# Optimization experiments

Hardware: AMD Instinct MI355X
Metric: run time of the kernel (lower is better)

## Reference

```python
import jax, jax.numpy as jnp
import numpy as np
from jax import lax

# ---- configuration (matches init_kwargs) ----
DH = 4.0        # grid_spacing (m)
DT = 0.0008     # time step (s), satisfies CFL for vmax=2600
PML = 20        # pml_width (cells, all four edges)
VMAX = 2600.0   # max_vel used for PML profile
PAD = 2         # halo for 4th-order (accuracy=4) stencil


def _shift(wp, k, axis, n):
    return lax.slice_in_dim(wp, PAD + k, PAD + k + n, axis=axis)


def _d1(w, axis, dh):
    # 4th-order first derivative: (-f[+2] + 8 f[+1] - 8 f[-1] + f[-2]) / (12 h)
    n = w.shape[axis]
    pad = [(0, 0)] * w.ndim
    pad[axis] = (PAD, PAD)
    wp = jnp.pad(w, pad)
    return ((_shift(wp, -2, axis, n) - _shift(wp, 2, axis, n))
            + 8.0 * (_shift(wp, 1, axis, n) - _shift(wp, -1, axis, n))) / (12.0 * dh)


def _d2(w, axis, dh):
    # 4th-order second derivative: (-f[+-2] + 16 f[+-1] - 30 f[0]) / (12 h^2)
    n = w.shape[axis]
    pad = [(0, 0)] * w.ndim
    pad[axis] = (PAD, PAD)
    wp = jnp.pad(w, pad)
    return (-(_shift(wp, -2, axis, n) + _shift(wp, 2, axis, n))
            + 16.0 * (_shift(wp, 1, axis, n) + _shift(wp, -1, axis, n))
            - 30.0 * w) / (12.0 * dh * dh)


def _pml_profiles(n, pml, dh, dt, vmax):
    # CPML absorption profiles: sigma ~ quadratic ramp into the PML,
    # b = exp(-sigma*dt), a = b - 1 (kappa=1, alpha=0)
    sigma_max = np.float32(3.0 * vmax * np.log(1000.0) / (2.0 * pml * dh))
    x = jnp.arange(n, dtype=jnp.float32)
    d = jnp.maximum(jnp.clip((pml - x) / pml, 0.0, 1.0),
                    jnp.clip((x - (n - 1 - pml)) / pml, 0.0, 1.0))
    sigma = sigma_max * d * d
    b = jnp.exp(-sigma * dt)
    return b - 1.0, b


def setup_inputs() -> dict:
    key = jax.random.key(0)
    k1, k2, k3, k4 = jax.random.split(key, 4)
    ny = nx = 400
    B, n_src, n_rec, nt = 4, 1, 100, 100
    v = 1500.0 + 1000.0 * jax.random.uniform(k1, (ny, nx), dtype=jnp.float32)
    source_amplitudes = jax.random.normal(k2, (B, n_src, nt), dtype=jnp.float32)
    source_locations = jax.random.randint(k3, (B, n_src, 2), 40, 360).astype(jnp.int64)
    receiver_locations = jax.random.randint(k4, (B, n_rec, 2), 40, 360).astype(jnp.int64)
    return {"v": v, "source_amplitudes": source_amplitudes,
            "source_locations": source_locations,
            "receiver_locations": receiver_locations}


def reference(v, source_amplitudes, source_locations, receiver_locations):
    B, n_src, nt = source_amplitudes.shape
    # replicate edge velocities into the PML region (as deepwave does)
    vp = jnp.pad(v, ((PML, PML), (PML, PML)), mode="edge")
    NY, NX = vp.shape
    v2dt2 = (vp * vp) * (DT * DT)          # [NY, NX]
    ay, by = _pml_profiles(NY, PML, DH, DT, VMAX)
    ax, bx = _pml_profiles(NX, PML, DH, DT, VMAX)
    ay, by = ay[None, :, None], by[None, :, None]
    ax, bx = ax[None, None, :], bx[None, None, :]

    sy = source_locations[..., 0] + PML    # [B, n_src]
    sx = source_locations[..., 1] + PML
    ry = receiver_locations[..., 0] + PML  # [B, n_rec]
    rx = receiver_locations[..., 1] + PML
    bidx = jnp.arange(B)[:, None]
    src_scale = v2dt2[sy, sx]              # [B, n_src]

    zero = jnp.zeros((B, NY, NX), v.dtype)
    carry0 = (zero, zero, zero, zero, zero, zero)

    def step(carry, amp_t):
        wfc, wfm, psiy, psix, zetay, zetax = carry
        # PML memory variables for first derivatives
        psiy = by * psiy + ay * _d1(wfc, 1, DH)
        psix = bx * psix + ax * _d1(wfc, 2, DH)
        # PML-corrected second derivatives
        d2y = _d2(wfc, 1, DH) + _d1(psiy, 1, DH)
        d2x = _d2(wfc, 2, DH) + _d1(psix, 2, DH)
        zetay = by * zetay + ay * d2y
        zetax = bx * zetax + ax * d2x
        # explicit leapfrog time step
        wfp = v2dt2[None] * (d2y + zetay + d2x + zetax) + 2.0 * wfc - wfm
        # inject sources scaled by v^2 dt^2 (as deepwave)
        wfp = wfp.at[bidx, sy, sx].add(src_scale * amp_t)
        rec = wfp[bidx, ry, rx]            # [B, n_rec]
        return (wfp, wfc, psiy, psix, zetay, zetax), rec

    amps_t = jnp.moveaxis(source_amplitudes, 2, 0)  # [nt, B, n_src]
    _, recs = lax.scan(step, carry0, amps_t)        # recs: [nt, B, n_rec]
    receiver_amplitudes = jnp.moveaxis(recs, 0, 2)  # [B, n_rec, nt]
    return receiver_amplitudes
```

## Files before the change

kernel.cpp:

```cpp
#include <hip/hip_runtime.h>

#define NVEL  400
#define PMLW  20
#define NSIDE 440
#define BATCH 4
#define NT    100
#define NREC  100

#define TS 55
#define GT 8
#define WP 65
#define PYP 56
#define PXP 60
#define ZP  56

#define C1f (1.0f/48.0f)
#define C2f (1.0f/192.0f)
#define NTH 1024

#define WIDX(y,x) (((y)+4)*WP + ((x)+4))

__global__ __launch_bounds__(NTH, 1) void kWave(
    const float* __restrict__ v, const float* __restrict__ amp,
    const int* __restrict__ sloc, const int* __restrict__ rloc,
    float* __restrict__ out, int* __restrict__ flags, float* __restrict__ strips)
{
    __shared__ float sWF0[63*WP], sWF1[63*WP];
    __shared__ float sPY[59*PYP];
    __shared__ float sPX[TS*PXP];
    __shared__ float sZY[TS*ZP], sZX[TS*ZP], sV2[TS*ZP];
    __shared__ float pa_y[63], pb_y[63], pa_x[63], pb_x[63];
    __shared__ float sAmp[NT];

    const int tid  = threadIdx.x;
    const int lane = tid & 63;
    const int wrow = tid >> 6;
    const int bid = blockIdx.x;
    const int b   = bid >> 6;
    const int tl  = bid & 63;
    const int tyi = tl >> 3, txi = tl & 7;
    const int by0 = tyi*TS, bx0 = txi*TS;
    const int nbN = (tyi > 0)    ? bid - GT : -1;
    const int nbS = (tyi < GT-1) ? bid + GT : -1;
    const int nbW = (txi > 0)    ? bid - 1  : -1;
    const int nbE = (txi < GT-1) ? bid + 1  : -1;

    for (int i = tid; i < 63*WP; i += NTH) { sWF0[i] = 0.f; sWF1[i] = 0.f; }
    for (int i = tid; i < 59*PYP; i += NTH) sPY[i] = 0.f;
    for (int i = tid; i < TS*PXP; i += NTH) sPX[i] = 0.f;
    for (int i = tid; i < TS*ZP; i += NTH) { sZY[i] = 0.f; sZX[i] = 0.f; }
    for (int i = tid; i < TS*TS; i += NTH) {
        int y = i/TS, x = i - y*TS;
        int cy = min(max(by0 + y - PMLW, 0), NVEL-1);
        int cx = min(max(bx0 + x - PMLW, 0), NVEL-1);
        float vv = v[cy*NVEL + cx];
        sV2[y*ZP + x] = vv*vv*(float)(0.0008*0.0008);
    }
    if (tid < 63) {
        const float smax = (float)(3.0*2600.0*6.907755278982137/160.0);
        float gy = (float)(by0 + tid - 4);
        float dy = fmaxf(fminf(fmaxf((20.f-gy)/20.f,0.f),1.f),
                         fminf(fmaxf((gy-419.f)/20.f,0.f),1.f));
        float bby = expf(-smax*dy*dy*0.0008f);
        pb_y[tid] = bby; pa_y[tid] = bby - 1.f;
        float gx = (float)(bx0 + tid - 4);
        float dx = fmaxf(fminf(fmaxf((20.f-gx)/20.f,0.f),1.f),
                         fminf(fmaxf((gx-419.f)/20.f,0.f),1.f));
        float bbx = expf(-smax*dx*dx*0.0008f);
        pb_x[tid] = bbx; pa_x[tid] = bbx - 1.f;
    }
    if (tid < NT) sAmp[tid] = amp[b*NT + tid];

    const int sly = sloc[b*2]   + PMLW - by0;
    const int slx = sloc[b*2+1] + PMLW - bx0;

    int rofs = -1, rIdx = 0;
    if (tid < NREC) {
        int gry = rloc[(b*NREC+tid)*2]   + PMLW;
        int grx = rloc[(b*NREC+tid)*2+1] + PMLW;
        if (gry >= by0 && gry < by0+TS && grx >= bx0 && grx < bx0+TS) {
            rofs = (b*NREC+tid)*NT;
            rIdx = WIDX(gry-by0, grx-bx0);
        }
    }

    int imp_nb = -1, imp_src = 0, imp_dst = 0, exp_src = 0;
    if (tid < 880) {
        int e = tid/220, j = tid - e*220;
        if (e == 0)      { int r=j/55, c=j-55*r; imp_nb=nbN; imp_src=1*220+j; imp_dst=WIDX(r-4,c);   exp_src=WIDX(r,c); }
        else if (e == 1) { int r=j/55, c=j-55*r; imp_nb=nbS; imp_src=0*220+j; imp_dst=WIDX(55+r,c);  exp_src=WIDX(51+r,c); }
        else if (e == 2) { int r=j&3,  c=j>>2;   imp_nb=nbW; imp_src=3*220+j; imp_dst=WIDX(c,r-4);   exp_src=WIDX(c,r); }
        else             { int r=j&3,  c=j>>2;   imp_nb=nbE; imp_src=2*220+j; imp_dst=WIDX(c,55+r);  exp_src=WIDX(c,51+r); }
    }
    __syncthreads();

    float* cur = sWF0;
    float* nxt = sWF1;

    for (int t = 0; t < NT; ++t) {
        if (t > 0 && imp_nb >= 0) {
            int spin = 0;
            while (__hip_atomic_load(&flags[imp_nb], __ATOMIC_RELAXED,
                                     __HIP_MEMORY_SCOPE_AGENT) < t
                   && spin < 2000000) { __builtin_amdgcn_s_sleep(1); ++spin; }
            asm volatile("" ::: "memory");
            cur[imp_dst] = __hip_atomic_load(
                &strips[(size_t)(((t-1)&1)*256 + imp_nb)*880 + imp_src],
                __ATOMIC_RELAXED, __HIP_MEMORY_SCOPE_AGENT);
        }
        __syncthreads();

        #pragma unroll
        for (int k = 0; k < 4; ++k) {
            int ri = wrow + 16*k;
            if (ri < 59 && lane < 55) {
                int r = ri - 2;
                int w = WIDX(r, lane);
                float d1 = (cur[w-2*WP] - cur[w+2*WP]
                            + 8.f*(cur[w+WP] - cur[w-WP])) * C1f;
                int gy = by0 + r;
                int pi = ri*PYP + lane;
                float val = 0.f;
                if (gy >= 0 && gy < NSIDE)
                    val = pb_y[r+4]*sPY[pi] + pa_y[r+4]*d1;
                sPY[pi] = val;
            }
        }
        #pragma unroll
        for (int k = 0; k < 4; ++k) {
            int y = wrow + 16*k;
            if (y < 55 && lane < 59) {
                int c = lane - 2;
                int w = WIDX(y, c);
                float d1 = (cur[w-2] - cur[w+2]
                            + 8.f*(cur[w+1] - cur[w-1])) * C1f;
                int gx = bx0 + c;
                int pi = y*PXP + lane;
                float val = 0.f;
                if (gx >= 0 && gx < NSIDE)
                    val = pb_x[c+4]*sPX[pi] + pa_x[c+4]*d1;
                sPX[pi] = val;
            }
        }
        __syncthreads();

        #pragma unroll
        for (int k = 0; k < 4; ++k) {
            int y = wrow + 16*k;
            if (y < 55 && lane < 55) {
                int x = lane;
                int w = WIDX(y, x);
                float wc = cur[w];
                float d2y = (-(cur[w-2*WP] + cur[w+2*WP])
                             + 16.f*(cur[w-WP] + cur[w+WP]) - 30.f*wc) * C2f
                          + (sPY[y*PYP+x] - sPY[(y+4)*PYP+x]
                             + 8.f*(sPY[(y+3)*PYP+x] - sPY[(y+1)*PYP+x])) * C1f;
                float d2x = (-(cur[w-2] + cur[w+2])
                             + 16.f*(cur[w-1] + cur[w+1]) - 30.f*wc) * C2f
                          + (sPX[y*PXP+x] - sPX[y*PXP+x+4]
                             + 8.f*(sPX[y*PXP+x+3] - sPX[y*PXP+x+1])) * C1f;
                int zi = y*ZP + x;
                float zy = pb_y[y+4]*sZY[zi] + pa_y[y+4]*d2y;
                float zx = pb_x[x+4]*sZX[zi] + pa_x[x+4]*d2x;
                sZY[zi] = zy; sZX[zi] = zx;
                float wnew = sV2[zi]*(d2y + zy + d2x + zx) + 2.f*wc - nxt[w];
                if (y == sly && x == slx) wnew += sV2[zi] * sAmp[t];
                nxt[w] = wnew;
            }
        }
        __syncthreads();

        if (rofs >= 0) out[rofs + t] = nxt[rIdx];
        if (t < NT-1) {
            if (tid < 880)
                __hip_atomic_store(&strips[(size_t)((t&1)*256 + bid)*880 + tid],
                                   nxt[exp_src], __ATOMIC_RELAXED,
                                   __HIP_MEMORY_SCOPE_AGENT);
            __builtin_amdgcn_s_waitcnt(0);
            __syncthreads();
            if (tid == 0)
                __hip_atomic_store(&flags[bid], t+1, __ATOMIC_RELEASE,
                                   __HIP_MEMORY_SCOPE_AGENT);
        }
        float* tmp = cur; cur = nxt; nxt = tmp;
    }
}

extern "C" void kernel_launch(void* const* d_in, const int* in_sizes, int n_in,
                              void* d_out, int out_size, void* d_ws, size_t ws_size,
                              hipStream_t stream) {
    const float* v    = (const float*)d_in[0];
    const float* amp  = (const float*)d_in[1];
    const int*   sloc = (const int*)d_in[2];
    const int*   rloc = (const int*)d_in[3];
    float* out = (float*)d_out;

    int*   flags  = (int*)d_ws;
    float* strips = (float*)((char*)d_ws + 1024);

    hipMemsetAsync(flags, 0, 1024, stream);
    kWave<<<256, NTH, 0, stream>>>(v, amp, sloc, rloc, out, flags, strips);
}
```

Before: 853.9 us.

## Vectorize stencil by float4, keep PML state in registers, overlap halo exchange with interior

Rewrites the per-step work so each thread handles four consecutive x-points using float4 LDS loads, and moves the zeta memory variables, v^2dt^2 and PML coefficients from shared memory into registers. Core psi updates now run before the halo import is written. The time step is split so boundary/rim points are computed first, then the waves owning them export strips and raise the neighbor flag while the remaining waves compute the interior. This aims to take the inter-block halo exchange and flag signalling off the critical path and to cut LDS traffic and instruction count. In exchange it adds complex thread-role partitioning and an LDS atomic counter for signalling, and it depends on the exported strip cells being exactly those finished in the early phase.

```diff
diff --git a/kernel.cpp b/kernel.cpp
--- a/kernel.cpp
+++ b/kernel.cpp
@@ -9,15 +9,19 @@
 
 #define TS 55
 #define GT 8
-#define WP 65
+#define WP 68
+#define WROWS 63
+#define WHALF (WROWS*WP)
 #define PYP 56
 #define PXP 60
-#define ZP  56
-
 #define C1f (1.0f/48.0f)
 #define C2f (1.0f/192.0f)
 #define NTH 1024
-
+#define NSTRIP 880
+#define SPITCH (256*NSTRIP)
+
+typedef float f4 __attribute__((ext_vector_type(4)));
+#define F4(x) (*(f4*)&(x))
 #define WIDX(y,x) (((y)+4)*WP + ((x)+4))
 
 __global__ __launch_bounds__(NTH, 1) void kWave(
@@ -25,16 +29,14 @@
     const int* __restrict__ sloc, const int* __restrict__ rloc,
     float* __restrict__ out, int* __restrict__ flags, float* __restrict__ strips)
 {
-    __shared__ float sWF0[63*WP], sWF1[63*WP];
-    __shared__ float sPY[59*PYP];
-    __shared__ float sPX[TS*PXP];
-    __shared__ float sZY[TS*ZP], sZX[TS*ZP], sV2[TS*ZP];
+    __shared__ __align__(16) float sWF[2*WHALF];
+    __shared__ __align__(16) float sPY[59*PYP];
+    __shared__ __align__(16) float sPX[TS*PXP];
     __shared__ float pa_y[63], pb_y[63], pa_x[63], pb_x[63];
     __shared__ float sAmp[NT];
-
-    const int tid  = threadIdx.x;
-    const int lane = tid & 63;
-    const int wrow = tid >> 6;
+    __shared__ int expCnt, initCnt;
+
+    const int tid = threadIdx.x;
     const int bid = blockIdx.x;
     const int b   = bid >> 6;
     const int tl  = bid & 63;
@@ -45,17 +47,10 @@
     const int nbW = (txi > 0)    ? bid - 1  : -1;
     const int nbE = (txi < GT-1) ? bid + 1  : -1;
 
-    for (int i = tid; i < 63*WP; i += NTH) { sWF0[i] = 0.f; sWF1[i] = 0.f; }
+    for (int i = tid; i < 2*WHALF; i += NTH) sWF[i] = 0.f;
     for (int i = tid; i < 59*PYP; i += NTH) sPY[i] = 0.f;
     for (int i = tid; i < TS*PXP; i += NTH) sPX[i] = 0.f;
-    for (int i = tid; i < TS*ZP; i += NTH) { sZY[i] = 0.f; sZX[i] = 0.f; }
-    for (int i = tid; i < TS*TS; i += NTH) {
-        int y = i/TS, x = i - y*TS;
-        int cy = min(max(by0 + y - PMLW, 0), NVEL-1);
-        int cx = min(max(bx0 + x - PMLW, 0), NVEL-1);
-        float vv = v[cy*NVEL + cx];
-        sV2[y*ZP + x] = vv*vv*(float)(0.0008*0.0008);
-    }
+    if (tid == 0) initCnt = 0;
     if (tid < 63) {
         const float smax = (float)(3.0*2600.0*6.907755278982137/160.0);
         float gy = (float)(by0 + tid - 4);
@@ -70,9 +65,56 @@
         pb_x[tid] = bbx; pa_x[tid] = bbx - 1.f;
     }
     if (tid < NT) sAmp[tid] = amp[b*NT + tid];
-
-    const int sly = sloc[b*2]   + PMLW - by0;
-    const int slx = sloc[b*2+1] + PMLW - bx0;
+    __syncthreads();
+
+    const bool pyOn = (tid < 826);
+    const int  pyRi = tid/14, pyQx = (tid - 14*pyRi)*4;
+    const bool pyCore = pyOn && (pyRi >= 4 && pyRi <= 54);
+    const bool pyRim  = pyOn && !(pyRi >= 4 && pyRi <= 54);
+    const int  pyWf  = pyRi*WP + (pyQx+4);
+    const int  pyIdx = pyRi*PYP + pyQx;
+    float pyPa = 0.f, pyPb = 0.f;
+    if (pyOn) { int g = by0 + pyRi - 2;
+        if (g >= 0 && g < NSIDE) { pyPa = pa_y[pyRi+2]; pyPb = pb_y[pyRi+2]; } }
+
+    const bool pxOn = (tid < 825);
+    const int  pxY = tid/15, pxQ = tid - 15*pxY, pxJ = pxQ*4;
+    const bool pxCore = pxOn && (pxQ >= 1 && pxQ <= 12);
+    const bool pxRim  = pxOn && !(pxQ >= 1 && pxQ <= 12);
+    const int  pxWf  = (pxY+4)*WP + pxJ;
+    const int  pxIdx = pxY*PXP + pxJ;
+    f4 pxPa, pxPb;
+    #pragma unroll
+    for (int e = 0; e < 4; ++e) {
+        int g = bx0 + pxJ - 2 + e;
+        bool ok = pxOn && (g >= 0 && g < NSIDE);
+        pxPa[e] = ok ? pa_x[pxJ+2+e] : 0.f;
+        pxPb[e] = ok ? pb_x[pxJ+2+e] : 0.f;
+    }
+
+    const bool inOn = (tid < 770);
+    const int  iY = tid/14, iQ = tid - 14*iY, iQx = iQ*4;
+    const bool iEarly = inOn && ((iY < 4) || (iY >= 51) || (iQ == 0) || (iQ == 13));
+    const bool iLate  = inOn && !((iY < 4) || (iY >= 51) || (iQ == 0) || (iQ == 13));
+    const bool iTail  = (iQ == 13);
+    const int  iC  = WIDX(iY, iQx);
+    const int  iPy = iY*PYP + iQx;
+    const int  iPx = iY*PXP + iQx;
+    const float iPay = pa_y[iY+4], iPby = pb_y[iY+4];
+    f4 iPax, iPbx, iV2, iSrc;
+    {
+        const int sgy = sloc[b*2] + PMLW, sgx = sloc[b*2+1] + PMLW;
+        #pragma unroll
+        for (int e = 0; e < 4; ++e) {
+            iPax[e] = pa_x[iQx+e+4]; iPbx[e] = pb_x[iQx+e+4];
+            int cy = min(max(by0 + iY  - PMLW, 0), NVEL-1);
+            int cx = min(max(bx0 + iQx+e - PMLW, 0), NVEL-1);
+            float vv = v[cy*NVEL + cx];
+            iV2[e] = vv*vv*(float)(0.0008*0.0008);
+            iSrc[e] = (inOn && (by0+iY == sgy) && (bx0+iQx+e == sgx)) ? iV2[e] : 0.f;
+        }
+    }
+    f4 zY = {0.f,0.f,0.f,0.f}, zX = {0.f,0.f,0.f,0.f};
 
     int rofs = -1, rIdx = 0;
     if (tid < NREC) {
@@ -84,106 +126,141 @@
         }
     }
 
-    int imp_nb = -1, imp_src = 0, imp_dst = 0, exp_src = 0;
-    if (tid < 880) {
+    int impNb = -1, imSrc = 0, imDst = 0;
+    if (tid < NSTRIP) {
         int e = tid/220, j = tid - e*220;
-        if (e == 0)      { int r=j/55, c=j-55*r; imp_nb=nbN; imp_src=1*220+j; imp_dst=WIDX(r-4,c);   exp_src=WIDX(r,c); }
-        else if (e == 1) { int r=j/55, c=j-55*r; imp_nb=nbS; imp_src=0*220+j; imp_dst=WIDX(55+r,c);  exp_src=WIDX(51+r,c); }
-        else if (e == 2) { int r=j&3,  c=j>>2;   imp_nb=nbW; imp_src=3*220+j; imp_dst=WIDX(c,r-4);   exp_src=WIDX(c,r); }
-        else             { int r=j&3,  c=j>>2;   imp_nb=nbE; imp_src=2*220+j; imp_dst=WIDX(c,55+r);  exp_src=WIDX(c,51+r); }
+        if (e == 0)      { int r=j/55, c=j-55*r; impNb=nbN; imSrc=1*220+j; imDst=WIDX(r-4,c); }
+        else if (e == 1) { int r=j/55, c=j-55*r; impNb=nbS; imSrc=0*220+j; imDst=WIDX(55+r,c); }
+        else if (e == 2) { int r=j&3,  c=j>>2;   impNb=nbW; imSrc=3*220+j; imDst=WIDX(c,r-4); }
+        else             { int r=j&3,  c=j>>2;   impNb=nbE; imSrc=2*220+j; imDst=WIDX(c,55+r); }
+        if (impNb >= 0) imSrc += impNb*NSTRIP;
+    }
+
+    const bool isFree = !iLate;
+    unsigned long long fb = __ballot(isFree ? 1 : 0);
+    const bool iFirstFree = isFree && ((tid & 63) == (__ffsll((long long)fb) - 1));
+    int es0 = -1, eg0 = 0, es1 = -1, eg1 = 0;
+    {
+        int er = -1;
+        if (isFree) er = atomicAdd(&initCnt, 1);
+        #pragma unroll
+        for (int s = 0; s < 2; ++s) {
+            int i = er + 460*s;
+            if (er >= 0 && i < NSTRIP) {
+                int e = i/220, j = i - e*220, src;
+                if (e == 0)      { int r=j/55, c=j-55*r; src = WIDX(r,c); }
+                else if (e == 1) { int r=j/55, c=j-55*r; src = WIDX(51+r,c); }
+                else if (e == 2) { int r=j&3,  c=j>>2;   src = WIDX(c,r); }
+                else             { int r=j&3,  c=j>>2;   src = WIDX(c,51+r); }
+                if (s == 0) { es0 = src; eg0 = bid*NSTRIP + i; }
+                else        { es1 = src; eg1 = bid*NSTRIP + i; }
+            }
+        }
     }
     __syncthreads();
 
-    float* cur = sWF0;
-    float* nxt = sWF1;
+    int co = 0;
+
+#define PSIY_BODY { \
+    f4 r0 = F4(sWF[co+pyWf]);      f4 r1 = F4(sWF[co+pyWf+WP]); \
+    f4 r3 = F4(sWF[co+pyWf+3*WP]); f4 r4 = F4(sWF[co+pyWf+4*WP]); \
+    f4 po = F4(sPY[pyIdx]); f4 nv; \
+    _Pragma("unroll") for (int e = 0; e < 4; ++e) { \
+        float d1 = (r0[e] - r4[e] + 8.f*(r3[e] - r1[e]))*C1f; \
+        nv[e] = pyPb*po[e] + pyPa*d1; } \
+    F4(sPY[pyIdx]) = nv; }
+
+#define PSIX_BODY { \
+    f4 L = F4(sWF[co+pxWf]); f4 R = F4(sWF[co+pxWf+4]); \
+    f4 po = F4(sPX[pxIdx]); f4 nv; \
+    float w8[8] = {L.x,L.y,L.z,L.w,R.x,R.y,R.z,R.w}; \
+    _Pragma("unroll") for (int e = 0; e < 4; ++e) { \
+        float d1 = (w8[e] - w8[e+4] + 8.f*(w8[e+3] - w8[e+1]))*C1f; \
+        nv[e] = pxPb[e]*po[e] + pxPa[e]*d1; } \
+    F4(sPX[pxIdx]) = nv; }
+
+#define INTERIOR_BODY { \
+    int cn = co ^ WHALF; \
+    f4 Cc  = F4(sWF[co+iC]); \
+    f4 ym2 = F4(sWF[co+iC-2*WP]), ym1 = F4(sWF[co+iC-WP]); \
+    f4 yp1 = F4(sWF[co+iC+WP]),  yp2 = F4(sWF[co+iC+2*WP]); \
+    f4 xl  = F4(sWF[co+iC-4]),   xr  = F4(sWF[co+iC+4]); \
+    f4 p0 = F4(sPY[iPy]),        p1 = F4(sPY[iPy+PYP]); \
+    f4 p3 = F4(sPY[iPy+3*PYP]),  p4 = F4(sPY[iPy+4*PYP]); \
+    f4 pl = F4(sPX[iPx]),        pr = F4(sPX[iPx+4]); \
+    f4 n4 = F4(sWF[cn+iC]); \
+    float xw[12] = {xl.x,xl.y,xl.z,xl.w,Cc.x,Cc.y,Cc.z,Cc.w,xr.x,xr.y,xr.z,xr.w}; \
+    float pw[8]  = {pl.x,pl.y,pl.z,pl.w,pr.x,pr.y,pr.z,pr.w}; \
+    float ampT = sAmp[t]; f4 w4; \
+    _Pragma("unroll") for (int e = 0; e < 4; ++e) { \
+        float d2y = (-(ym2[e]+yp2[e]) + 16.f*(ym1[e]+yp1[e]) - 30.f*Cc[e])*C2f \
+                  + (p0[e] - p4[e] + 8.f*(p3[e] - p1[e]))*C1f; \
+        float d2x = (-(xw[2+e]+xw[6+e]) + 16.f*(xw[3+e]+xw[5+e]) - 30.f*xw[4+e])*C2f \
+                  + (pw[e] - pw[e+4] + 8.f*(pw[e+3] - pw[e+1]))*C1f; \
+        float zy = iPby*zY[e] + iPay*d2y; \
+        float zx = iPbx[e]*zX[e] + iPax[e]*d2x; \
+        zY[e] = zy; zX[e] = zx; \
+        w4[e] = iV2[e]*(d2y + zy + d2x + zx) + 2.f*Cc[e] - n4[e] + iSrc[e]*ampT; } \
+    if (!iTail) F4(sWF[cn+iC]) = w4; \
+    else { sWF[cn+iC] = w4.x; sWF[cn+iC+1] = w4.y; sWF[cn+iC+2] = w4.z; } }
 
     for (int t = 0; t < NT; ++t) {
-        if (t > 0 && imp_nb >= 0) {
+        if (tid == 0) expCnt = 0;
+        float hval = 0.f;
+        if (t > 0 && impNb >= 0) {
             int spin = 0;
-            while (__hip_atomic_load(&flags[imp_nb], __ATOMIC_RELAXED,
+            while (__hip_atomic_load(&flags[impNb], __ATOMIC_RELAXED,
                                      __HIP_MEMORY_SCOPE_AGENT) < t
                    && spin < 2000000) { __builtin_amdgcn_s_sleep(1); ++spin; }
-            asm volatile("" ::: "memory");
-            cur[imp_dst] = __hip_atomic_load(
-                &strips[(size_t)(((t-1)&1)*256 + imp_nb)*880 + imp_src],
-                __ATOMIC_RELAXED, __HIP_MEMORY_SCOPE_AGENT);
-        }
-        __syncthreads();
-
-        #pragma unroll
-        for (int k = 0; k < 4; ++k) {
-            int ri = wrow + 16*k;
-            if (ri < 59 && lane < 55) {
-                int r = ri - 2;
-                int w = WIDX(r, lane);
-                float d1 = (cur[w-2*WP] - cur[w+2*WP]
-                            + 8.f*(cur[w+WP] - cur[w-WP])) * C1f;
-                int gy = by0 + r;
-                int pi = ri*PYP + lane;
-                float val = 0.f;
-                if (gy >= 0 && gy < NSIDE)
-                    val = pb_y[r+4]*sPY[pi] + pa_y[r+4]*d1;
-                sPY[pi] = val;
+            hval = __hip_atomic_load(&strips[((t-1)&1)*SPITCH + imSrc],
+                                     __ATOMIC_RELAXED, __HIP_MEMORY_SCOPE_AGENT);
+        }
+        asm volatile("" ::: "memory");
+
+        if (pyCore) PSIY_BODY;
+        if (pxCore) PSIX_BODY;
+
+        if (t > 0 && impNb >= 0) sWF[co+imDst] = hval;
+        __syncthreads();
+
+        if (pyRim) PSIY_BODY;
+        if (pxRim) PSIX_BODY;
+        __syncthreads();
+
+        if (iEarly) INTERIOR_BODY;
+        __syncthreads();
+
+        if (isFree) {
+            if (t < NT-1) {
+                int cn = co ^ WHALF;
+                float g0 = (es0 >= 0) ? sWF[cn+es0] : 0.f;
+                float g1 = (es1 >= 0) ? sWF[cn+es1] : 0.f;
+                int pb = (t&1)*SPITCH;
+                if (es0 >= 0)
+                    __hip_atomic_store(&strips[pb+eg0], g0, __ATOMIC_RELAXED,
+                                       __HIP_MEMORY_SCOPE_AGENT);
+                if (es1 >= 0)
+                    __hip_atomic_store(&strips[pb+eg1], g1, __ATOMIC_RELAXED,
+                                       __HIP_MEMORY_SCOPE_AGENT);
+                __builtin_amdgcn_s_waitcnt(0);
+                if (iFirstFree) {
+                    if (atomicAdd(&expCnt, 1) == 15)
+                        __hip_atomic_store(&flags[bid], t+1, __ATOMIC_RELEASE,
+                                           __HIP_MEMORY_SCOPE_AGENT);
+                }
             }
-        }
-        #pragma unroll
-        for (int k = 0; k < 4; ++k) {
-            int y = wrow + 16*k;
-            if (y < 55 && lane < 59) {
-                int c = lane - 2;
-                int w = WIDX(y, c);
-                float d1 = (cur[w-2] - cur[w+2]
-                            + 8.f*(cur[w+1] - cur[w-1])) * C1f;
-                int gx = bx0 + c;
-                int pi = y*PXP + lane;
-                float val = 0.f;
-                if (gx >= 0 && gx < NSIDE)
-                    val = pb_x[c+4]*sPX[pi] + pa_x[c+4]*d1;
-                sPX[pi] = val;
-            }
-        }
-        __syncthreads();
-
-        #pragma unroll
-        for (int k = 0; k < 4; ++k) {
-            int y = wrow + 16*k;
-            if (y < 55 && lane < 55) {
-                int x = lane;
-                int w = WIDX(y, x);
-                float wc = cur[w];
-                float d2y = (-(cur[w-2*WP] + cur[w+2*WP])
-                             + 16.f*(cur[w-WP] + cur[w+WP]) - 30.f*wc) * C2f
-                          + (sPY[y*PYP+x] - sPY[(y+4)*PYP+x]
-                             + 8.f*(sPY[(y+3)*PYP+x] - sPY[(y+1)*PYP+x])) * C1f;
-                float d2x = (-(cur[w-2] + cur[w+2])
-                             + 16.f*(cur[w-1] + cur[w+1]) - 30.f*wc) * C2f
-                          + (sPX[y*PXP+x] - sPX[y*PXP+x+4]
-                             + 8.f*(sPX[y*PXP+x+3] - sPX[y*PXP+x+1])) * C1f;
-                int zi = y*ZP + x;
-                float zy = pb_y[y+4]*sZY[zi] + pa_y[y+4]*d2y;
-                float zx = pb_x[x+4]*sZX[zi] + pa_x[x+4]*d2x;
-                sZY[zi] = zy; sZX[zi] = zx;
-                float wnew = sV2[zi]*(d2y + zy + d2x + zx) + 2.f*wc - nxt[w];
-                if (y == sly && x == slx) wnew += sV2[zi] * sAmp[t];
-                nxt[w] = wnew;
-            }
-        }
-        __syncthreads();
-
-        if (rofs >= 0) out[rofs + t] = nxt[rIdx];
-        if (t < NT-1) {
-            if (tid < 880)
-                __hip_atomic_store(&strips[(size_t)((t&1)*256 + bid)*880 + tid],
-                                   nxt[exp_src], __ATOMIC_RELAXED,
-                                   __HIP_MEMORY_SCOPE_AGENT);
-            __builtin_amdgcn_s_waitcnt(0);
-            __syncthreads();
-            if (tid == 0)
-                __hip_atomic_store(&flags[bid], t+1, __ATOMIC_RELEASE,
-                                   __HIP_MEMORY_SCOPE_AGENT);
-        }
-        float* tmp = cur; cur = nxt; nxt = tmp;
-    }
+        } else {
+            INTERIOR_BODY;
+        }
+        __syncthreads();
+
+        if (rofs >= 0) out[rofs + t] = sWF[(co^WHALF) + rIdx];
+
+        co ^= WHALF;
+    }
+#undef PSIY_BODY
+#undef PSIX_BODY
+#undef INTERIOR_BODY
 }
 
 extern "C" void kernel_launch(void* const* d_in, const int* in_sizes, int n_in,
```

Result: slower. 1.182 ms (+38.4%).
